# Kernel tuning notes

Hardware: AMD Instinct MI355X
Metric: run time of the kernel (lower is better)

Reference implementation:

```python
import jax, jax.numpy as jnp
import numpy as np

H_HEADS = 32
KV_HEADS = 8
HEAD_DIM = 128
HIDDEN = 2048
EPS = 1e-6


def rms_norm(x, w):
    # normalize over last dim (head_dim)
    var = jnp.mean(jnp.square(x), axis=-1, keepdims=True)
    return x * jax.lax.rsqrt(var + EPS) * w


def rotate_half(x):
    x1, x2 = jnp.split(x, 2, axis=-1)
    return jnp.concatenate([-x2, x1], axis=-1)


def setup_inputs() -> dict:
    key = jax.random.key(0)
    ks = jax.random.split(key, 8)
    B, Q, CTX = 1, 1024, 2048
    T = CTX + Q
    hidden_states = jax.random.normal(ks[0], (B, Q, HIDDEN), jnp.float32)
    target_hidden = jax.random.normal(ks[1], (B, CTX, HIDDEN), jnp.float32)
    # RoPE tables over the full concatenated length
    inv_freq = 1.0 / (10000.0 ** (np.arange(0, HEAD_DIM, 2, dtype=np.float32) / HEAD_DIM))
    pos = np.arange(T, dtype=np.float32)
    freqs = np.outer(pos, inv_freq)                     # [T, hd/2]
    emb = np.concatenate([freqs, freqs], axis=-1)       # [T, hd]
    cos = jnp.asarray(np.cos(emb))[None]                # [1, T, hd]
    sin = jnp.asarray(np.sin(emb))[None]
    # custom mask: context fully visible, causal within noise block
    noise_causal = jnp.tril(jnp.ones((Q, Q), bool))
    mask = jnp.concatenate([jnp.ones((Q, CTX), bool), noise_causal], axis=1)
    attention_mask = mask[None, None]                   # [1,1,Q,T]
    scale = 0.02
    wq = jax.random.normal(ks[2], (H_HEADS * HEAD_DIM, HIDDEN), jnp.float32) * scale
    wk = jax.random.normal(ks[3], (KV_HEADS * HEAD_DIM, HIDDEN), jnp.float32) * scale
    wv = jax.random.normal(ks[4], (KV_HEADS * HEAD_DIM, HIDDEN), jnp.float32) * scale
    wo = jax.random.normal(ks[5], (HIDDEN, H_HEADS * HEAD_DIM), jnp.float32) * scale
    q_norm_w = jnp.ones((HEAD_DIM,), jnp.float32)
    k_norm_w = jnp.ones((HEAD_DIM,), jnp.float32)
    return {"hidden_states": hidden_states, "target_hidden": target_hidden,
            "cos": cos, "sin": sin, "attention_mask": attention_mask,
            "wq": wq, "wk": wk, "wv": wv, "wo": wo,
            "q_norm_w": q_norm_w, "k_norm_w": k_norm_w}


def reference(hidden_states, target_hidden, cos, sin, attention_mask,
              wq, wk, wv, wo, q_norm_w, k_norm_w):
    B, Q, _ = hidden_states.shape
    CTX = target_hidden.shape[1]
    T = CTX + Q
    n_rep = H_HEADS // KV_HEADS
    scaling = HEAD_DIM ** -0.5

    # Q from noise tokens, QK-RMSNorm per head
    q = (hidden_states @ wq.T).reshape(B, Q, H_HEADS, HEAD_DIM)
    q = rms_norm(q, q_norm_w).transpose(0, 2, 1, 3)          # [B,H,Q,hd]

    # K/V: context then noise, concatenated along sequence
    k = jnp.concatenate([target_hidden @ wk.T, hidden_states @ wk.T], axis=1)
    k = rms_norm(k.reshape(B, T, KV_HEADS, HEAD_DIM), k_norm_w).transpose(0, 2, 1, 3)  # [B,Hk,T,hd]
    v = jnp.concatenate([target_hidden @ wv.T, hidden_states @ wv.T], axis=1)
    v = v.reshape(B, T, KV_HEADS, HEAD_DIM).transpose(0, 2, 1, 3)                       # [B,Hk,T,hd]

    # offset RoPE: K uses all T positions, Q uses the last Q positions
    cos_b = cos[:, None]                                      # [B,1,T,hd]
    sin_b = sin[:, None]
    q = q * cos_b[:, :, -Q:, :] + rotate_half(q) * sin_b[:, :, -Q:, :]
    k = k * cos_b + rotate_half(k) * sin_b

    # GQA attention without materializing repeated K/V
    qg = q.reshape(B, KV_HEADS, n_rep, Q, HEAD_DIM)
    scores = jnp.einsum('bgrqd,bgtd->bgrqt', qg, k) * scaling  # [B,Hk,rep,Q,T]
    scores = jnp.where(attention_mask[:, :, None], scores, jnp.finfo(scores.dtype).min)
    probs = jax.nn.softmax(scores, axis=-1)
    out = jnp.einsum('bgrqt,bgtd->bgrqd', probs, v)            # [B,Hk,rep,Q,hd]
    out = out.reshape(B, H_HEADS, Q, HEAD_DIM).transpose(0, 2, 1, 3).reshape(B, Q, H_HEADS * HEAD_DIM)
    return out @ wo.T
```

## Files before the change

kernel.cpp:

```cpp
#include <hip/hip_runtime.h>

#define HIDDEN 2048
#define NQ     1024
#define NCTX   2048
#define NTOT   3072
#define NHEADS 32
#define KVH    8
#define HD     128

typedef __attribute__((ext_vector_type(8))) __bf16 bf16x8;
typedef __attribute__((ext_vector_type(4))) __bf16 bf16x4;
typedef __attribute__((ext_vector_type(4))) float  f32x4;

#define MFMA16(a, b, c) __builtin_amdgcn_mfma_f32_16x16x32_bf16(a, b, c, 0, 0, 0)

#define MSTATIC 12.0f

__device__ __forceinline__ void load_lds16(const void* g, void* l) {
    __builtin_amdgcn_global_load_lds(
        (const __attribute__((address_space(1))) unsigned int*)g,
        (__attribute__((address_space(3))) unsigned int*)l, 16, 0, 0);
}

__global__ __launch_bounds__(256) void conv4_f32_bf16(const float* __restrict__ s0,
                                                      __bf16* __restrict__ d0, int n0,
                                                      const float* __restrict__ s1,
                                                      __bf16* __restrict__ d1, int n1,
                                                      const float* __restrict__ s2,
                                                      __bf16* __restrict__ d2, int n2,
                                                      const float* __restrict__ s3,
                                                      __bf16* __restrict__ d3, int n3) {
    const float* s; __bf16* d; int n;
    switch (blockIdx.y) {
        case 0:  s = s0; d = d0; n = n0; break;
        case 1:  s = s1; d = d1; n = n1; break;
        case 2:  s = s2; d = d2; n = n2; break;
        default: s = s3; d = d3; n = n3; break;
    }
    int i = blockIdx.x * 256 + threadIdx.x;
    int stride = gridDim.x * 256;
    for (; i < n; i += stride) {
        float4 v = ((const float4*)s)[i];
        bf16x4 o;
        o[0] = (__bf16)v.x; o[1] = (__bf16)v.y;
        o[2] = (__bf16)v.z; o[3] = (__bf16)v.w;
        ((bf16x4*)d)[i] = o;
    }
}

__device__ __forceinline__ void gemm_compute256(const __bf16 (&As)[256][64],
                                                const __bf16 (&Bs)[64][64],
                                                f32x4 (&acc)[4][4],
                                                int wm, int n16, int quad, int rx) {
#pragma unroll
    for (int ks = 0; ks < 2; ks++) {
        bf16x8 af[4], bfr[4];
#pragma unroll
        for (int i = 0; i < 4; i++)
            af[i] = *(const bf16x8*)&As[wm + i * 16 + n16][((ks * 4 + quad) ^ rx) * 8];
#pragma unroll
        for (int j = 0; j < 4; j++)
            bfr[j] = *(const bf16x8*)&Bs[j * 16 + n16][((ks * 4 + quad) ^ rx) * 8];
#pragma unroll
        for (int i = 0; i < 4; i++)
#pragma unroll
            for (int j = 0; j < 4; j++)
                acc[i][j] = MFMA16(af[i], bfr[j], acc[i][j]);
    }
}

template <typename OutT>
__device__ __forceinline__ void gemm_epi256(const f32x4 (&acc)[4][4],
                                            OutT* __restrict__ Cblk, int ldc,
                                            int wm, int n16, int quad) {
#pragma unroll
    for (int i = 0; i < 4; i++)
#pragma unroll
        for (int j = 0; j < 4; j++)
#pragma unroll
            for (int r = 0; r < 4; r++)
                Cblk[(long)(wm + i * 16 + quad * 4 + r) * ldc + j * 16 + n16] =
                    (OutT)acc[i][j][r];
}

template <typename OutT>
__device__ __forceinline__ void gemm25664_bb(__bf16 (&As)[256][64], __bf16 (&Bs)[64][64],
                                             const __bf16* __restrict__ Ablk,
                                             const __bf16* __restrict__ Bblk,
                                             OutT* __restrict__ Cblk,
                                             int K, int lda, int ldb, int ldc) {
    const int tid  = threadIdx.x;
    const int lane = tid & 63;
    const int w    = tid >> 6;
    const int n16  = lane & 15;
    const int quad = lane >> 4;
    const int wm   = w * 64;

    f32x4 acc[4][4];
    const f32x4 fzero = {0.f, 0.f, 0.f, 0.f};
#pragma unroll
    for (int i = 0; i < 4; i++)
#pragma unroll
        for (int j = 0; j < 4; j++) acc[i][j] = fzero;

    const int arow  = w * 64 + (lane >> 3);
    const int brow  = w * 16 + (lane >> 3);
    const int sxor  = (lane >> 3) & 7;
    const int scol  = (lane & 7) * 8;
    const int sgcol = ((lane & 7) ^ sxor) * 8;
    const __bf16* Ap = Ablk + (long)arow * lda + sgcol;
    const __bf16* Bp = Bblk + (long)brow * ldb + sgcol;
    const int rx = n16 & 7;

    for (int k0 = 0; k0 < K; k0 += 64) {
#pragma unroll
        for (int i = 0; i < 8; i++)
            load_lds16(Ap + (long)i * 8 * lda + k0, &As[arow + i * 8][scol]);
#pragma unroll
        for (int i = 0; i < 2; i++)
            load_lds16(Bp + (long)i * 8 * ldb + k0, &Bs[brow + i * 8][scol]);
        __syncthreads();
        gemm_compute256(As, Bs, acc, wm, n16, quad, rx);
        __syncthreads();
    }
    gemm_epi256(acc, Cblk, ldc, wm, n16, quad);
}

template <typename OutT>
__device__ __forceinline__ void gemm25664_fb(__bf16 (&As)[256][64], __bf16 (&Bs)[64][64],
                                             const __bf16* __restrict__ Ablk,
                                             const float* __restrict__ Bblk,
                                             OutT* __restrict__ Cblk,
                                             int K, int lda, int ldb, int ldc) {
    const int tid  = threadIdx.x;
    const int lane = tid & 63;
    const int w    = tid >> 6;
    const int n16  = lane & 15;
    const int quad = lane >> 4;
    const int wm   = w * 64;

    f32x4 acc[4][4];
    const f32x4 fzero = {0.f, 0.f, 0.f, 0.f};
#pragma unroll
    for (int i = 0; i < 4; i++)
#pragma unroll
        for (int j = 0; j < 4; j++) acc[i][j] = fzero;

    const int arow  = w * 64 + (lane >> 3);
    const int sxor  = (lane >> 3) & 7;
    const int scol  = (lane & 7) * 8;
    const int sgcol = ((lane & 7) ^ sxor) * 8;
    const __bf16* Ap = Ablk + (long)arow * lda + sgcol;

    const int brr  = tid >> 2;
    const int bc0  = (tid & 3) * 16;
    const int bch  = (tid & 3) * 2;
    const int bxor = brr & 7;
    const float* Bptr = Bblk + (long)brr * ldb + bc0;

    const int rx = n16 & 7;
    float4 breg[4];

#define LOAD_B(kk)                                                             \
    _Pragma("unroll") for (int i = 0; i < 4; i++)                              \
        breg[i] = *(const float4*)(Bptr + (kk) + i * 4);

    LOAD_B(0);
    for (int k0 = 0; k0 < K; k0 += 64) {
#pragma unroll
        for (int i = 0; i < 8; i++)
            load_lds16(Ap + (long)i * 8 * lda + k0, &As[arow + i * 8][scol]);
        {
            bf16x8 b0, b1;
#pragma unroll
            for (int j = 0; j < 4; j++) {
                b0[j]     = (__bf16)breg[0][j]; b0[j + 4] = (__bf16)breg[1][j];
                b1[j]     = (__bf16)breg[2][j]; b1[j + 4] = (__bf16)breg[3][j];
            }
            *(bf16x8*)&Bs[brr][((bch + 0) ^ bxor) * 8] = b0;
            *(bf16x8*)&Bs[brr][((bch + 1) ^ bxor) * 8] = b1;
        }
        if (k0 + 64 < K) LOAD_B(k0 + 64);
        __syncthreads();
        gemm_compute256(As, Bs, acc, wm, n16, quad, rx);
        __syncthreads();
    }
#undef LOAD_B
    gemm_epi256(acc, Cblk, ldc, wm, n16, quad);
}

__global__ __launch_bounds__(256, 4) void gemm_kvq(const __bf16* __restrict__ tgtb,
                                                   const __bf16* __restrict__ hidb,
                                                   const __bf16* __restrict__ wkb,
                                                   const __bf16* __restrict__ wvb,
                                                   const float* __restrict__ wq,
                                                   __bf16* __restrict__ kbf,
                                                   __bf16* __restrict__ vbf,
                                                   __bf16* __restrict__ qbf) {
    __shared__ __bf16 As[256][64];
    __shared__ __bf16 Bs[64][64];
    const int bid = blockIdx.x;
    const int b = (bid & 7) * 80 + (bid >> 3);
    if (b < 384) {
        const int z = b >= 192, t = b - z * 192;
        const int m0 = (t >> 4) * 256, n0 = (t & 15) * 64;
        const __bf16* Ap = (m0 < 2048) ? tgtb + (long)m0 * 2048
                                       : hidb + (long)(m0 - 2048) * 2048;
        const __bf16* Bp = (z ? wvb : wkb) + (long)n0 * 2048;
        __bf16* Cp = (z ? vbf : kbf) + (long)m0 * 1024 + n0;
        gemm25664_bb<__bf16>(As, Bs, Ap, Bp, Cp, 2048, 2048, 2048, 1024);
    } else {
        const int t = b - 384;
        const int m0 = (t >> 6) * 256, n0 = (t & 63) * 64;
        gemm25664_fb<__bf16>(As, Bs, hidb + (long)m0 * 2048, wq + (long)n0 * 2048,
                             qbf + (long)m0 * 4096 + n0, 2048, 2048, 2048, 4096);
    }
}

__global__ __launch_bounds__(256, 4) void gemm_wo4(const __bf16* __restrict__ A,
                                                   const float* __restrict__ wo,
                                                   float* __restrict__ out,
                                                   float* __restrict__ p1,
                                                   float* __restrict__ p2,
                                                   float* __restrict__ p3) {
    __shared__ __bf16 As[256][64];
    __shared__ __bf16 Bs[64][64];
    const int bid = blockIdx.x;
    const int b = (bid & 7) * 64 + (bid >> 3);
    const int z = b >> 7, t = b & 127;
    const int m0 = (t >> 5) * 256, n0 = (t & 31) * 64;
    float* C;
    switch (z) {
        case 0:  C = out; break;
        case 1:  C = p1;  break;
        case 2:  C = p2;  break;
        default: C = p3;  break;
    }
    gemm25664_fb<float>(As, Bs, A + (long)m0 * 4096 + z * 1024,
                        wo + (long)n0 * 4096 + z * 1024,
                        C + (long)m0 * 2048 + n0, 1024, 4096, 4096, 2048);
}

__global__ __launch_bounds__(256) void add4_wo(float* __restrict__ out,
                                               const float* __restrict__ p1,
                                               const float* __restrict__ p2,
                                               const float* __restrict__ p3, int n4) {
    int i = blockIdx.x * 256 + threadIdx.x;
    int stride = gridDim.x * 256;
    for (; i < n4; i += stride) {
        float4 a = ((const float4*)out)[i];
        float4 b = ((const float4*)p1)[i];
        float4 c = ((const float4*)p2)[i];
        float4 d = ((const float4*)p3)[i];
        float4 o;
        o.x = (a.x + b.x) + (c.x + d.x);
        o.y = (a.y + b.y) + (c.y + d.y);
        o.z = (a.z + b.z) + (c.z + d.z);
        o.w = (a.w + b.w) + (c.w + d.w);
        ((float4*)out)[i] = o;
    }
}

__global__ __launch_bounds__(256) void rmsnorm_rope2(__bf16* __restrict__ xq,
                                                     const float* __restrict__ wq,
                                                     __bf16* __restrict__ xk,
                                                     const float* __restrict__ wk,
                                                     const float* __restrict__ cosb,
                                                     const float* __restrict__ sinb) {
    const int z = blockIdx.y;
    __bf16*      x = z ? xk : xq;
    const float* w = z ? wk : wq;
    const int nheads     = z ? 8 : 32;
    const int row_stride = z ? 1024 : 4096;
    const int pos_offset = z ? 0 : 2048;
    const float outscale = z ? 1.0f : 0.08838834764831845f;
    const int nitems     = z ? 3072 * 8 : 1024 * 32;

    int item = blockIdx.x * 4 + (threadIdx.x >> 6);
    int lane = threadIdx.x & 63;
    if (item >= nitems) return;
    int row = item / nheads;
    int head = item - row * nheads;
    __bf16* p = x + (long)row * row_stride + head * HD;

    float x1 = (float)p[lane], x2 = (float)p[lane + 64];
    float ss = x1 * x1 + x2 * x2;
#pragma unroll
    for (int o = 32; o >= 1; o >>= 1) ss += __shfl_xor(ss, o);
    float r = rsqrtf(ss * (1.0f / 128.0f) + 1e-6f) * outscale;

    int pos = pos_offset + row;
    float c1 = cosb[pos * HD + lane], c2 = cosb[pos * HD + lane + 64];
    float s1 = sinb[pos * HD + lane], s2 = sinb[pos * HD + lane + 64];
    float y1 = x1 * r * w[lane];
    float y2 = x2 * r * w[lane + 64];
    p[lane]      = (__bf16)(y1 * c1 - y2 * s1);
    p[lane + 64] = (__bf16)(y2 * c2 + y1 * s2);
}

__global__ __launch_bounds__(256) void transpose_v(const __bf16* __restrict__ v,
                                                   __bf16* __restrict__ vt) {
    __shared__ __bf16 T[64][68];
    const int tid = threadIdx.x;
    const int t0 = blockIdx.x * 64;
    const int d0 = blockIdx.y * 64;
    const int g  = blockIdx.z;
    const __bf16* src = v + (long)t0 * 1024 + g * 128 + d0;
#pragma unroll
    for (int i = 0; i < 4; i++) {
        int idx = tid + i * 256;
        int r = idx >> 4, c4 = (idx & 15) * 4;
        *(bf16x4*)&T[r][c4] = *(const bf16x4*)(src + (long)r * 1024 + c4);
    }
    __syncthreads();
    __bf16* dst = vt + (long)g * 128 * 3072 + (long)d0 * 3072 + t0;
#pragma unroll
    for (int i = 0; i < 4; i++) {
        int idx = tid + i * 256;
        int r = idx >> 4, c4 = (idx & 15) * 4;
        bf16x4 o;
        o[0] = T[c4 + 0][r]; o[1] = T[c4 + 1][r];
        o[2] = T[c4 + 2][r]; o[3] = T[c4 + 3][r];
        *(bf16x4*)(dst + (long)r * 3072 + c4) = o;
    }
}

__global__ __launch_bounds__(256) void flash_attn_splitk(const __bf16* __restrict__ qb,
                                                         const __bf16* __restrict__ kb,
                                                         const __bf16* __restrict__ vtg,
                                                         __bf16* __restrict__ Opart0,
                                                         __bf16* __restrict__ Opart1,
                                                         __bf16* __restrict__ Opart2,
                                                         float* __restrict__ lsum) {
    __shared__ __bf16 KsU[64 * 136];
    __shared__ __bf16 Vs[128][72];
    __shared__ __bf16 PsU[4 * 32 * 68];
#define KS(r, c) KsU[(r) * 136 + (c)]
#define PS(w_, m_, t_) PsU[(w_) * 2176 + (m_) * 68 + (t_)]

    const int tid  = threadIdx.x;
    const int lane = tid & 63;
    const int w    = tid >> 6;
    const int n    = lane & 15;
    const int quad = lane >> 4;

    const int bid = blockIdx.x;
    const int s   = blockIdx.y;
    const int g  = bid & 7;
    const int jj = bid >> 3;
    const int h  = g * 4 + (jj & 3);
    const int qt = jj >> 2;

    const int qr0 = qt * 128 + w * 16;

    bf16x8 qf[2][4];
#pragma unroll
    for (int mt = 0; mt < 2; mt++) {
        const __bf16* qp = qb + (long)(qr0 + mt * 64 + n) * 4096 + h * 128 + quad * 8;
        qf[mt][0] = *(const bf16x8*)(qp);
        qf[mt][1] = *(const bf16x8*)(qp + 32);
        qf[mt][2] = *(const bf16x8*)(qp + 64);
        qf[mt][3] = *(const bf16x8*)(qp + 96);
    }

    f32x4 O[2][8];
    const f32x4 fzero = {0.f, 0.f, 0.f, 0.f};
#pragma unroll
    for (int mt = 0; mt < 2; mt++)
#pragma unroll
        for (int dt = 0; dt < 8; dt++) O[mt][dt] = fzero;
    float l_loc[2] = {0.f, 0.f};

    const int ntot = 34 + 2 * qt;
    const int tbeg = (s * ntot) / 3;
    const int tend = ((s + 1) * ntot) / 3;

    const int krr = tid >> 4, kc8 = (tid & 15) * 8;
    const int vrr = tid >> 3, vc8 = (tid & 7) * 8;
    const __bf16* kp = kb + g * 128 + (long)(tbeg * 64 + krr) * 1024 + kc8;
    const __bf16* vp = vtg + (long)g * 128 * 3072 + (long)vrr * 3072 + tbeg * 64 + vc8;

    for (int tt = tbeg; tt < tend; tt++) {
#pragma unroll
        for (int i = 0; i < 4; i++)
            *(bf16x8*)&KS(krr + i * 16, kc8) = *(const bf16x8*)(kp + (long)i * 16 * 1024);
#pragma unroll
        for (int i = 0; i < 4; i++)
            *(bf16x8*)&Vs[vrr + i * 32][vc8] = *(const bf16x8*)(vp + (long)i * 32 * 3072);
        kp += 64 * 1024;
        vp += 64;
        __syncthreads();

        f32x4 S[2][4];
#pragma unroll
        for (int nt = 0; nt < 4; nt++) {
            f32x4 a0 = fzero, a1 = fzero;
#pragma unroll
            for (int ks = 0; ks < 4; ks++) {
                bf16x8 kf = *(const bf16x8*)&KS(nt * 16 + n, ks * 32 + quad * 8);
                a0 = MFMA16(kf, qf[0][ks], a0);
                a1 = MFMA16(kf, qf[1][ks], a1);
            }
            S[0][nt] = a0;
            S[1][nt] = a1;
        }

        if (tt >= ntot - 2) {
            const int t0 = tt * 64;
#pragma unroll
            for (int mt = 0; mt < 2; mt++) {
                const int lim = 2048 + qr0 + mt * 64 + n;
#pragma unroll
                for (int nt = 0; nt < 4; nt++)
#pragma unroll
                    for (int r = 0; r < 4; r++) {
                        int t = t0 + nt * 16 + quad * 4 + r;
                        if (t > lim) S[mt][nt][r] = -1e30f;
                    }
            }
        }

#pragma unroll
        for (int mt = 0; mt < 2; mt++)
#pragma unroll
            for (int nt = 0; nt < 4; nt++)
#pragma unroll
                for (int r = 0; r < 4; r++) {
                    float p = __expf(S[mt][nt][r] - MSTATIC);
                    S[mt][nt][r] = p;
                    l_loc[mt] += p;
                }

#pragma unroll
        for (int mt = 0; mt < 2; mt++)
#pragma unroll
            for (int nt = 0; nt < 4; nt++) {
                bf16x4 pk;
#pragma unroll
                for (int r = 0; r < 4; r++) pk[r] = (__bf16)S[mt][nt][r];
                *(bf16x4*)&PS(w, mt * 16 + n, nt * 16 + quad * 4) = pk;
            }

        bf16x8 pa[2][2];
#pragma unroll
        for (int mt = 0; mt < 2; mt++)
#pragma unroll
            for (int kg = 0; kg < 2; kg++)
                pa[mt][kg] = *(const bf16x8*)&PS(w, mt * 16 + n, kg * 32 + quad * 8);

#pragma unroll
        for (int dt = 0; dt < 8; dt++) {
            bf16x8 vf0 = *(const bf16x8*)&Vs[dt * 16 + n][quad * 8];
            bf16x8 vf1 = *(const bf16x8*)&Vs[dt * 16 + n][32 + quad * 8];
#pragma unroll
            for (int mt = 0; mt < 2; mt++) {
                f32x4 acc = O[mt][dt];
                acc = MFMA16(pa[mt][0], vf0, acc);
                acc = MFMA16(pa[mt][1], vf1, acc);
                O[mt][dt] = acc;
            }
        }

        __syncthreads();
    }

#pragma unroll
    for (int mt = 0; mt < 2; mt++) {
        float sm = l_loc[mt];
        sm += __shfl_xor(sm, 16);
        sm += __shfl_xor(sm, 32);
        l_loc[mt] = sm;
    }

    __bf16* Op = (s == 0) ? Opart0 : (s == 1 ? Opart1 : Opart2);
    const long tb = (long)(h * 8 + qt) * 128 * 128;
#pragma unroll
    for (int mt = 0; mt < 2; mt++)
#pragma unroll
        for (int dt = 0; dt < 8; dt++)
#pragma unroll
            for (int r = 0; r < 4; r++)
                Op[tb + (long)(mt * 64 + w * 16 + quad * 4 + r) * 128 + dt * 16 + n] =
                    (__bf16)O[mt][dt][r];
    if (quad == 0) {
        const int lb = (s * 256 + h * 8 + qt) * 128 + w * 16;
#pragma unroll
        for (int mt = 0; mt < 2; mt++)
            lsum[lb + mt * 64 + n] = l_loc[mt];
    }
#undef KS
#undef PS
}

__global__ __launch_bounds__(256) void flash_merge(const __bf16* __restrict__ O0,
                                                   const __bf16* __restrict__ O1,
                                                   const __bf16* __restrict__ O2,
                                                   const float* __restrict__ lsum,
                                                   __bf16* __restrict__ ob) {
    const int bx = blockIdx.x;
    const int h   = bx >> 4;
    const int r6  = bx & 15;
    const int qt  = r6 >> 1;
    const int sub = r6 & 1;
    const int row  = threadIdx.x >> 2;
    const int cseg = (threadIdx.x & 3) * 32;
    const int mrow = sub * 64 + row;

    const int tilei = h * 8 + qt;
    float inv = 1.0f / (lsum[tilei * 128 + mrow] + lsum[(256 + tilei) * 128 + mrow] +
                        lsum[(512 + tilei) * 128 + mrow]);

    const long src = (long)tilei * 128 * 128 + (long)mrow * 128 + cseg;
    __bf16* dst = ob + (long)(qt * 128 + mrow) * 4096 + h * 128 + cseg;
#pragma unroll
    for (int j = 0; j < 4; j++) {
        bf16x8 x0 = *(const bf16x8*)(O0 + src + j * 8);
        bf16x8 x1 = *(const bf16x8*)(O1 + src + j * 8);
        bf16x8 x2 = *(const bf16x8*)(O2 + src + j * 8);
        bf16x8 o;
#pragma unroll
        for (int k = 0; k < 8; k++)
            o[k] = (__bf16)((((float)x0[k] + (float)x1[k]) + (float)x2[k]) * inv);
        *(bf16x8*)(dst + j * 8) = o;
    }
}

extern "C" void kernel_launch(void* const* d_in, const int* in_sizes, int n_in,
                              void* d_out, int out_size, void* d_ws, size_t ws_size,
                              hipStream_t stream) {
    const float* hidden = (const float*)d_in[0];
    const float* target = (const float*)d_in[1];
    const float* cosb   = (const float*)d_in[2];
    const float* sinb   = (const float*)d_in[3];
    const float* wq = (const float*)d_in[5];
    const float* wk = (const float*)d_in[6];
    const float* wv = (const float*)d_in[7];
    const float* wo = (const float*)d_in[8];
    const float* qw = (const float*)d_in[9];
    const float* kw = (const float*)d_in[10];
    float* out = (float*)d_out;

    char* ws = (char*)d_ws;
    const long MB = 1 << 20;
    __bf16* kbf  = (__bf16*)(ws);
    __bf16* vtg  = (__bf16*)(ws + 6 * MB);
    __bf16* vbf  = (__bf16*)(ws + 12 * MB);
    __bf16* hidb = (__bf16*)(ws + 20 * MB);
    __bf16* tgtb = (__bf16*)(ws + 24 * MB);
    __bf16* wkb  = (__bf16*)(ws + 32 * MB);
    __bf16* wvb  = (__bf16*)(ws + 36 * MB);
    __bf16* Op0  = (__bf16*)(ws + 12 * MB);
    __bf16* Op1  = (__bf16*)(ws + 20 * MB);
    __bf16* Op2  = (__bf16*)(ws + 28 * MB);
    float*  lbuf = (float*)(ws + 36 * MB);
    __bf16* attnb= (__bf16*)(ws);
    float*  po1  = (float*)(ws + 8 * MB);
    float*  po2  = (float*)(ws + 16 * MB);
    float*  po3  = (float*)(ws + 24 * MB);
    __bf16* qbf  = (__bf16*)d_out;

    dim3 blk(256);

    conv4_f32_bf16<<<dim3(1024, 4), blk, 0, stream>>>(
        hidden, hidb, (1024 * 2048) / 4, target, tgtb, (2048 * 2048) / 4,
        wk, wkb, (1024 * 2048) / 4, wv, wvb, (1024 * 2048) / 4);

    gemm_kvq<<<640, blk, 0, stream>>>(tgtb, hidb, wkb, wvb, wq, kbf, vbf, qbf);

    rmsnorm_rope2<<<dim3(8192, 2), blk, 0, stream>>>(qbf, qw, kbf, kw, cosb, sinb);

    transpose_v<<<dim3(48, 2, 8), blk, 0, stream>>>(vbf, vtg);

    flash_attn_splitk<<<dim3(256, 3), blk, 0, stream>>>(qbf, kbf, vtg,
                                                        Op0, Op1, Op2, lbuf);
    flash_merge<<<512, blk, 0, stream>>>(Op0, Op1, Op2, lbuf, attnb);

    gemm_wo4<<<512, blk, 0, stream>>>(attnb, wo, out, po1, po2, po3);
    add4_wo<<<1024, blk, 0, stream>>>(out, po1, po2, po3, (1024 * 2048) / 4);
}
```

Baseline: 344.4 us.

## Fuse V transpose into GEMM epilogue and use two-way attention split

The V projection GEMM now writes its output directly in transposed [group][dim][token] layout, so the separate transpose_v kernel and its round trip through global memory go away. The flash attention split-K is also cut from three key ranges to two. That means fewer blocks, fewer partial outputs, and a cheaper merge step. The cost is that the transposed epilogue stores are strided 4-element writes, and with only 512 attention blocks the GPU may be less well filled and the causal tiles less evenly balanced.

Result: faster. 337.3 us (-2.1%).

```diff
diff --git a/kernel.cpp b/kernel.cpp
--- a/kernel.cpp
+++ b/kernel.cpp
@@ -83,25 +83,33 @@
                     (OutT)acc[i][j][r];
 }
 
-template <typename OutT>
-__device__ __forceinline__ void gemm25664_bb(__bf16 (&As)[256][64], __bf16 (&Bs)[64][64],
-                                             const __bf16* __restrict__ Ablk,
-                                             const __bf16* __restrict__ Bblk,
-                                             OutT* __restrict__ Cblk,
-                                             int K, int lda, int ldb, int ldc) {
+__device__ __forceinline__ void gemm_epi256_vT(const f32x4 (&acc)[4][4],
+                                               __bf16* __restrict__ base,
+                                               int m0, int wm, int n16, int quad) {
+#pragma unroll
+    for (int i = 0; i < 4; i++)
+#pragma unroll
+        for (int j = 0; j < 4; j++) {
+            bf16x4 o;
+#pragma unroll
+            for (int r = 0; r < 4; r++) o[r] = (__bf16)acc[i][j][r];
+            *(bf16x4*)(base + (long)(j * 16 + n16) * 3072 +
+                       (m0 + wm + i * 16 + quad * 4)) = o;
+        }
+}
+
+__device__ __forceinline__ void gemm25664_bb_core(__bf16 (&As)[256][64],
+                                                  __bf16 (&Bs)[64][64],
+                                                  const __bf16* __restrict__ Ablk,
+                                                  const __bf16* __restrict__ Bblk,
+                                                  f32x4 (&acc)[4][4],
+                                                  int K, int lda, int ldb) {
     const int tid  = threadIdx.x;
     const int lane = tid & 63;
     const int w    = tid >> 6;
     const int n16  = lane & 15;
     const int quad = lane >> 4;
     const int wm   = w * 64;
-
-    f32x4 acc[4][4];
-    const f32x4 fzero = {0.f, 0.f, 0.f, 0.f};
-#pragma unroll
-    for (int i = 0; i < 4; i++)
-#pragma unroll
-        for (int j = 0; j < 4; j++) acc[i][j] = fzero;
 
     const int arow  = w * 64 + (lane >> 3);
     const int brow  = w * 16 + (lane >> 3);
@@ -123,7 +131,6 @@
         gemm_compute256(As, Bs, acc, wm, n16, quad, rx);
         __syncthreads();
     }
-    gemm_epi256(acc, Cblk, ldc, wm, n16, quad);
 }
 
 template <typename OutT>
@@ -195,10 +202,17 @@
                                                    const __bf16* __restrict__ wvb,
                                                    const float* __restrict__ wq,
                                                    __bf16* __restrict__ kbf,
-                                                   __bf16* __restrict__ vbf,
+                                                   __bf16* __restrict__ vtg,
                                                    __bf16* __restrict__ qbf) {
     __shared__ __bf16 As[256][64];
     __shared__ __bf16 Bs[64][64];
+    const int tid  = threadIdx.x;
+    const int lane = tid & 63;
+    const int w    = tid >> 6;
+    const int n16  = lane & 15;
+    const int quad = lane >> 4;
+    const int wm   = w * 64;
+
     const int bid = blockIdx.x;
     const int b = (bid & 7) * 80 + (bid >> 3);
     if (b < 384) {
@@ -207,8 +221,19 @@
         const __bf16* Ap = (m0 < 2048) ? tgtb + (long)m0 * 2048
                                        : hidb + (long)(m0 - 2048) * 2048;
         const __bf16* Bp = (z ? wvb : wkb) + (long)n0 * 2048;
-        __bf16* Cp = (z ? vbf : kbf) + (long)m0 * 1024 + n0;
-        gemm25664_bb<__bf16>(As, Bs, Ap, Bp, Cp, 2048, 2048, 2048, 1024);
+        f32x4 acc[4][4];
+        const f32x4 fzero = {0.f, 0.f, 0.f, 0.f};
+#pragma unroll
+        for (int i = 0; i < 4; i++)
+#pragma unroll
+            for (int j = 0; j < 4; j++) acc[i][j] = fzero;
+        gemm25664_bb_core(As, Bs, Ap, Bp, acc, 2048, 2048, 2048);
+        if (z) {
+            __bf16* base = vtg + (long)(n0 >> 7) * 128 * 3072 + (long)(n0 & 127) * 3072;
+            gemm_epi256_vT(acc, base, m0, wm, n16, quad);
+        } else {
+            gemm_epi256<__bf16>(acc, kbf + (long)m0 * 1024 + n0, 1024, wm, n16, quad);
+        }
     } else {
         const int t = b - 384;
         const int m0 = (t >> 6) * 256, n0 = (t & 63) * 64;
@@ -298,39 +323,11 @@
     p[lane + 64] = (__bf16)(y2 * c2 + y1 * s2);
 }
 
-__global__ __launch_bounds__(256) void transpose_v(const __bf16* __restrict__ v,
-                                                   __bf16* __restrict__ vt) {
-    __shared__ __bf16 T[64][68];
-    const int tid = threadIdx.x;
-    const int t0 = blockIdx.x * 64;
-    const int d0 = blockIdx.y * 64;
-    const int g  = blockIdx.z;
-    const __bf16* src = v + (long)t0 * 1024 + g * 128 + d0;
-#pragma unroll
-    for (int i = 0; i < 4; i++) {
-        int idx = tid + i * 256;
-        int r = idx >> 4, c4 = (idx & 15) * 4;
-        *(bf16x4*)&T[r][c4] = *(const bf16x4*)(src + (long)r * 1024 + c4);
-    }
-    __syncthreads();
-    __bf16* dst = vt + (long)g * 128 * 3072 + (long)d0 * 3072 + t0;
-#pragma unroll
-    for (int i = 0; i < 4; i++) {
-        int idx = tid + i * 256;
-        int r = idx >> 4, c4 = (idx & 15) * 4;
-        bf16x4 o;
-        o[0] = T[c4 + 0][r]; o[1] = T[c4 + 1][r];
-        o[2] = T[c4 + 2][r]; o[3] = T[c4 + 3][r];
-        *(bf16x4*)(dst + (long)r * 3072 + c4) = o;
-    }
-}
-
 __global__ __launch_bounds__(256) void flash_attn_splitk(const __bf16* __restrict__ qb,
                                                          const __bf16* __restrict__ kb,
                                                          const __bf16* __restrict__ vtg,
                                                          __bf16* __restrict__ Opart0,
                                                          __bf16* __restrict__ Opart1,
-                                                         __bf16* __restrict__ Opart2,
                                                          float* __restrict__ lsum) {
     __shared__ __bf16 KsU[64 * 136];
     __shared__ __bf16 Vs[128][72];
@@ -372,8 +369,9 @@
     float l_loc[2] = {0.f, 0.f};
 
     const int ntot = 34 + 2 * qt;
-    const int tbeg = (s * ntot) / 3;
-    const int tend = ((s + 1) * ntot) / 3;
+    const int half = ntot >> 1;
+    const int tbeg = s ? half : 0;
+    const int tend = s ? ntot : half;
 
     const int krr = tid >> 4, kc8 = (tid & 15) * 8;
     const int vrr = tid >> 3, vc8 = (tid & 7) * 8;
@@ -472,7 +470,7 @@
         l_loc[mt] = sm;
     }
 
-    __bf16* Op = (s == 0) ? Opart0 : (s == 1 ? Opart1 : Opart2);
+    __bf16* Op = s ? Opart1 : Opart0;
     const long tb = (long)(h * 8 + qt) * 128 * 128;
 #pragma unroll
     for (int mt = 0; mt < 2; mt++)
@@ -494,7 +492,6 @@
 
 __global__ __launch_bounds__(256) void flash_merge(const __bf16* __restrict__ O0,
                                                    const __bf16* __restrict__ O1,
-                                                   const __bf16* __restrict__ O2,
                                                    const float* __restrict__ lsum,
                                                    __bf16* __restrict__ ob) {
     const int bx = blockIdx.x;
@@ -507,8 +504,7 @@
     const int mrow = sub * 64 + row;
 
     const int tilei = h * 8 + qt;
-    float inv = 1.0f / (lsum[tilei * 128 + mrow] + lsum[(256 + tilei) * 128 + mrow] +
-                        lsum[(512 + tilei) * 128 + mrow]);
+    float inv = 1.0f / (lsum[tilei * 128 + mrow] + lsum[(256 + tilei) * 128 + mrow]);
 
     const long src = (long)tilei * 128 * 128 + (long)mrow * 128 + cseg;
     __bf16* dst = ob + (long)(qt * 128 + mrow) * 4096 + h * 128 + cseg;
@@ -516,11 +512,10 @@
     for (int j = 0; j < 4; j++) {
         bf16x8 x0 = *(const bf16x8*)(O0 + src + j * 8);
         bf16x8 x1 = *(const bf16x8*)(O1 + src + j * 8);
-        bf16x8 x2 = *(const bf16x8*)(O2 + src + j * 8);
         bf16x8 o;
 #pragma unroll
         for (int k = 0; k < 8; k++)
-            o[k] = (__bf16)((((float)x0[k] + (float)x1[k]) + (float)x2[k]) * inv);
+            o[k] = (__bf16)(((float)x0[k] + (float)x1[k]) * inv);
         *(bf16x8*)(dst + j * 8) = o;
     }
 }
@@ -544,19 +539,17 @@
     const long MB = 1 << 20;
     __bf16* kbf  = (__bf16*)(ws);
     __bf16* vtg  = (__bf16*)(ws + 6 * MB);
-    __bf16* vbf  = (__bf16*)(ws + 12 * MB);
     __bf16* hidb = (__bf16*)(ws + 20 * MB);
     __bf16* tgtb = (__bf16*)(ws + 24 * MB);
     __bf16* wkb  = (__bf16*)(ws + 32 * MB);
     __bf16* wvb  = (__bf16*)(ws + 36 * MB);
     __bf16* Op0  = (__bf16*)(ws + 12 * MB);
     __bf16* Op1  = (__bf16*)(ws + 20 * MB);
-    __bf16* Op2  = (__bf16*)(ws + 28 * MB);
     float*  lbuf = (float*)(ws + 36 * MB);
     __bf16* attnb= (__bf16*)(ws);
     float*  po1  = (float*)(ws + 8 * MB);
     float*  po2  = (float*)(ws + 16 * MB);
-    float*  po3  = (float*)(ws + 24 * MB);
+    float*  po3  = (float*)(ws + 28 * MB);
     __bf16* qbf  = (__bf16*)d_out;
 
     dim3 blk(256);
@@ -565,15 +558,13 @@
         hidden, hidb, (1024 * 2048) / 4, target, tgtb, (2048 * 2048) / 4,
         wk, wkb, (1024 * 2048) / 4, wv, wvb, (1024 * 2048) / 4);
 
-    gemm_kvq<<<640, blk, 0, stream>>>(tgtb, hidb, wkb, wvb, wq, kbf, vbf, qbf);
+    gemm_kvq<<<640, blk, 0, stream>>>(tgtb, hidb, wkb, wvb, wq, kbf, vtg, qbf);
 
     rmsnorm_rope2<<<dim3(8192, 2), blk, 0, stream>>>(qbf, qw, kbf, kw, cosb, sinb);
 
-    transpose_v<<<dim3(48, 2, 8), blk, 0, stream>>>(vbf, vtg);
-
-    flash_attn_splitk<<<dim3(256, 3), blk, 0, stream>>>(qbf, kbf, vtg,
-                                                        Op0, Op1, Op2, lbuf);
-    flash_merge<<<512, blk, 0, stream>>>(Op0, Op1, Op2, lbuf, attnb);
+    flash_attn_splitk<<<dim3(256, 2), blk, 0, stream>>>(qbf, kbf, vtg,
+                                                        Op0, Op1, lbuf);
+    flash_merge<<<512, blk, 0, stream>>>(Op0, Op1, lbuf, attnb);
 
     gemm_wo4<<<512, blk, 0, stream>>>(attnb, wo, out, po1, po2, po3);
     add4_wo<<<1024, blk, 0, stream>>>(out, po1, po2, po3, (1024 * 2048) / 4);
```
